# Kernel tuning notes

Hardware: AMD Instinct MI355X
Metric: run time of the kernel (lower is better)

## Reference

```python
import jax, jax.numpy as jnp
import numpy as np

N = 65536      # total nodes (64 graphs x 1024 nodes)
E = 1048576    # total edges
B = 64         # graphs in the batch
H = 128        # in_dim == hidden_dim
HEAD = 4
EPS = 1e-5


def setup_inputs() -> dict:
    key = jax.random.key(0)
    ks = jax.random.split(key, 16)
    s = 0.02
    return {
        "h": jax.random.normal(ks[0], (N, H), jnp.float32),
        "inter_f": jax.random.normal(ks[1], (B, H), jnp.float32),
        "gamma1": jnp.ones((H,), jnp.float32), "beta1": jnp.zeros((H,), jnp.float32),
        "W1": jax.random.normal(ks[2], (H, H), jnp.float32) * s, "b1": jnp.zeros((H,), jnp.float32),
        "gamma2": jnp.ones((H,), jnp.float32), "beta2": jnp.zeros((H,), jnp.float32),
        "W2": jax.random.normal(ks[3], (H, H), jnp.float32) * s, "b2": jnp.zeros((H,), jnp.float32),
        "Wq": jax.random.normal(ks[4], (HEAD, H, H), jnp.float32) * s,
        "Wk": jax.random.normal(ks[5], (HEAD, H, H), jnp.float32) * s,
        "Wv": jax.random.normal(ks[6], (HEAD, H, H), jnp.float32) * s,
        "Wc": jax.random.normal(ks[7], (HEAD * H, H), jnp.float32) * s,
        "ln_g": jnp.ones((H,), jnp.float32), "ln_b": jnp.zeros((H,), jnp.float32),
        "Wf1": jax.random.normal(ks[8], (H, 2 * H), jnp.float32) * s, "bf1": jnp.zeros((2 * H,), jnp.float32),
        "Wf2": jax.random.normal(ks[9], (2 * H, H), jnp.float32) * s, "bf2": jnp.zeros((H,), jnp.float32),
        "src": jax.random.randint(ks[10], (E,), 0, N, jnp.int32),
        "dst": jax.random.randint(ks[11], (E,), 0, N, jnp.int32),
        "graph_id": (jnp.arange(N) // (N // B)).astype(jnp.int32),
    }


def _bn(x, g, b):
    # BatchNorm1d (training-mode batch statistics, biased var)
    m = x.mean(0)
    v = jnp.mean((x - m) ** 2, 0)
    return (x - m) * jax.lax.rsqrt(v + EPS) * g + b


def _ln(x, g, b):
    m = x.mean(-1, keepdims=True)
    v = jnp.mean((x - m) ** 2, -1, keepdims=True)
    return (x - m) * jax.lax.rsqrt(v + EPS) * g + b


def _gconv(x, W, b, src, dst):
    # dgl GraphConv, norm='both': D_out^{-1/2} gather -> scatter-add -> D_in^{-1/2}, then W, b
    ones_e = jnp.ones((E,), x.dtype)
    dout = jnp.maximum(jax.ops.segment_sum(ones_e, src, num_segments=N), 1.0)
    din = jnp.maximum(jax.ops.segment_sum(ones_e, dst, num_segments=N), 1.0)
    msg = (x * jax.lax.rsqrt(dout)[:, None])[src]            # [E, H] gather
    agg = jax.ops.segment_sum(msg, dst, num_segments=N)      # [N, H] scatter-add
    agg = agg * jax.lax.rsqrt(din)[:, None]
    return agg @ W + b


def _forward(h, inter_f, gamma1, beta1, W1, b1, gamma2, beta2, W2, b2,
             Wq, Wk, Wv, Wc, ln_g, ln_b, Wf1, bf1, Wf2, bf2, src, dst, graph_id):
    # init pooling (mean_nodes)
    counts = jax.ops.segment_sum(jnp.ones((N,), h.dtype), graph_id, num_segments=B)
    init_avg_h = jax.ops.segment_sum(h, graph_id, num_segments=B) / counts[:, None]

    # two residual GraphConv blocks (dropout is identity at inference)
    h1 = h + jax.nn.relu(_gconv(_bn(h, gamma1, beta1), W1, b1, src, dst))
    h2 = h1 + jax.nn.relu(_gconv(_bn(h1, gamma2, beta2), W2, b2, src, dst))

    # broadcast_nodes(inter_f)
    inter_h = inter_f[graph_id]                               # [N, H]

    # transformer_block: per-head q/k/v, per-node scalar att, per-graph segment softmax
    q = jnp.einsum('nd,hdo->hno', h2, Wq)
    k = jnp.einsum('nd,hdo->hno', inter_h, Wk)
    v = jnp.einsum('nd,hdo->hno', h2, Wv)
    att = jnp.sum(q * k, axis=-1) / jnp.sqrt(jnp.float32(1280.0))   # [HEAD, N]
    mx = jax.vmap(lambda a: jax.ops.segment_max(a, graph_id, num_segments=B))(att)  # [HEAD, B]
    e = jnp.exp(att - mx[:, graph_id])
    ssum = jax.vmap(lambda a: jax.ops.segment_sum(a, graph_id, num_segments=B))(e)
    alpha = e / ssum[:, graph_id]                             # segment softmax per head
    tp = v * alpha[..., None]                                 # [HEAD, N, H]
    mo = tp.transpose(1, 0, 2).reshape(N, HEAD * H) @ Wc      # concat heads + project

    x1 = _ln(mo + h2, ln_g, ln_b)
    x2 = _ln(jax.nn.relu(x1 @ Wf1 + bf1) @ Wf2 + bf2 + x1, ln_g, ln_b)

    readout = jax.ops.segment_sum(x2, graph_id, num_segments=B)     # sum_nodes
    return readout, init_avg_h


def reference(h, inter_f, gamma1, beta1, W1, b1, gamma2, beta2, W2, b2,
              Wq, Wk, Wv, Wc, ln_g, ln_b, Wf1, bf1, Wf2, bf2, src, dst, graph_id):
    return _forward(h, inter_f, gamma1, beta1, W1, b1, gamma2, beta2, W2, b2,
                    Wq, Wk, Wv, Wc, ln_g, ln_b, Wf1, bf1, Wf2, bf2, src, dst, graph_id)
```

## Files before the change

kernel.cpp:

```cpp
#include <hip/hip_runtime.h>

#define NN 65536
#define NE 1048576
#define NB 64
#define HD 128
#define HD2 256
#define NHEAD 4
#define NPG 1024
#define BEPS 1e-5f
#define BM 64
#define ESTRIDE 20480

typedef short bf16x8s __attribute__((ext_vector_type(8)));
typedef float f32x4 __attribute__((ext_vector_type(4)));
#define MFMA16(a,b,c) __builtin_amdgcn_mfma_f32_16x16x32_bf16(a,b,c,0,0,0)

__device__ __forceinline__ unsigned short f2bf(float f) {
    union { float f; unsigned int u; } x{f};
    unsigned int r = x.u + 0x7FFFu + ((x.u >> 16) & 1u);
    return (unsigned short)(r >> 16);
}
__device__ __forceinline__ float b2f(unsigned short s) {
    union { unsigned int u; float f; } x{((unsigned int)s) << 16};
    return x.f;
}

__global__ __launch_bounds__(1024) void k_prep_pool(const int* __restrict__ src, const int* __restrict__ dst,
                                                    int* __restrict__ gcurD, int* __restrict__ gcurS,
                                                    unsigned int* __restrict__ dbuck, unsigned short* __restrict__ sbuck,
                                                    const float* __restrict__ h,
                                                    float* __restrict__ psum, float* __restrict__ psq) {
    const int t = threadIdx.x;
    if (blockIdx.x < 64) {
        __shared__ int cntD[64], cntS[64], baseD[64], baseS[64];
        if (t < 64) { cntD[t] = 0; cntS[t] = 0; }
        __syncthreads();
        const int e0 = blockIdx.x * 16384;
        int sv[16], dv[16];
        #pragma unroll
        for (int j = 0; j < 16; ++j) {
            int e = e0 + j * 1024 + t;
            sv[j] = src[e]; dv[j] = dst[e];
            atomicAdd(&cntD[dv[j] >> 10], 1);
            atomicAdd(&cntS[sv[j] >> 10], 1);
        }
        __syncthreads();
        if (t < 64) baseD[t] = atomicAdd(&gcurD[t * 32], cntD[t]);
        else if (t < 128) baseS[t - 64] = atomicAdd(&gcurS[(t - 64) * 32], cntS[t - 64]);
        __syncthreads();
        if (t < 64) { cntD[t] = 0; cntS[t] = 0; }
        __syncthreads();
        #pragma unroll
        for (int j = 0; j < 16; ++j) {
            int gd = dv[j] >> 10;
            int slot = baseD[gd] + atomicAdd(&cntD[gd], 1);
            if (slot < ESTRIDE)
                dbuck[gd * ESTRIDE + slot] = (unsigned)(dv[j] & 1023) | ((unsigned)sv[j] << 10);
            int gs = sv[j] >> 10;
            int slot2 = baseS[gs] + atomicAdd(&cntS[gs], 1);
            if (slot2 < ESTRIDE)
                sbuck[gs * ESTRIDE + slot2] = (unsigned short)(sv[j] & 1023);
        }
    } else {
        __shared__ float ls[1024], lq[1024];
        const int bb = blockIdx.x - 64;
        const int r0 = bb * 256;
        const int c = t & 127, strip8 = t >> 7;
        float s = 0.f, sq = 0.f;
        for (int i = 0; i < 32; ++i) {
            float v = h[(size_t)(r0 + strip8 * 32 + i) * HD + c];
            s += v; sq += v * v;
        }
        ls[t] = s; lq[t] = sq;
        __syncthreads();
        if (t < 128) {
            float ss = 0.f, qq = 0.f;
            #pragma unroll
            for (int k = 0; k < 8; ++k) { ss += ls[t + k * 128]; qq += lq[t + k * 128]; }
            psum[bb * HD + t] = ss;
            psq[bb * HD + t]  = qq;
        }
    }
}

__global__ __launch_bounds__(1024) void k_prep2(const int* __restrict__ gcurD, const int* __restrict__ gcurS,
                                                const unsigned int* __restrict__ dbuck,
                                                const unsigned short* __restrict__ sbuck,
                                                float* __restrict__ din_r, float* __restrict__ dout_r,
                                                int* __restrict__ beg, int* __restrict__ endv,
                                                int* __restrict__ elist) {
    __shared__ int hist[1024];
    __shared__ int pre[1024];
    const int t = threadIdx.x;
    const int b = blockIdx.x;
    if (b < 64) {
        const int g = b;
        const int n = min(gcurD[g * 32], ESTRIDE);
        const unsigned int* pd = dbuck + g * ESTRIDE;
        hist[t] = 0;
        __syncthreads();
        for (int i = t; i < n; i += 1024) atomicAdd(&hist[pd[i] & 1023], 1);
        __syncthreads();
        const int cnt = hist[t];
        din_r[g * 1024 + t] = rsqrtf((float)max(cnt, 1));
        int x = cnt; pre[t] = x;
        __syncthreads();
        #pragma unroll
        for (int off = 1; off < 1024; off <<= 1) {
            int v = (t >= off) ? pre[t - off] : 0;
            __syncthreads();
            x += v; pre[t] = x;
            __syncthreads();
        }
        const int excl = x - cnt;
        beg[g * 1024 + t]  = g * ESTRIDE + excl;
        endv[g * 1024 + t] = g * ESTRIDE + excl + cnt;
        __syncthreads();
        hist[t] = excl; pre[t] = 0;
        __syncthreads();
        for (int i = t; i < n; i += 1024) {
            unsigned int w = pd[i];
            int dl = w & 1023;
            int r = atomicAdd(&pre[dl], 1);
            elist[g * ESTRIDE + hist[dl] + r] = (int)(w >> 10);
        }
    } else {
        const int g = b - 64;
        const int m = min(gcurS[g * 32], ESTRIDE);
        const unsigned short* ps = sbuck + g * ESTRIDE;
        hist[t] = 0;
        __syncthreads();
        for (int i = t; i < m; i += 1024) atomicAdd(&hist[ps[i]], 1);
        __syncthreads();
        dout_r[g * 1024 + t] = rsqrtf((float)max(hist[t], 1));
    }
}

__device__ __forceinline__ void dev_prepW(int idx, const float* __restrict__ W,
                                          unsigned short* __restrict__ frag, int O) {
    int l = idx & 63, tt = idx >> 6;
    int ot = O >> 4;
    int c = tt % ot, ks = tt / ot;
    int q = l >> 4, m = l & 15;
    const float* wp = W + (size_t)(ks * 32 + q * 8) * O + c * 16 + m;
    union { uint4 v; unsigned short u[8]; } pk;
    #pragma unroll
    for (int j = 0; j < 8; ++j) pk.u[j] = f2bf(wp[(size_t)j * O]);
    *(uint4*)(frag + (size_t)idx * 8) = pk.v;
}

__global__ __launch_bounds__(256) void k_wprep(const float* __restrict__ W1, const float* __restrict__ W2,
                                               const float* __restrict__ Wf1, const float* __restrict__ Wf2,
                                               const float* __restrict__ interf, const float* __restrict__ Wk,
                                               const float* __restrict__ Wq, const float* __restrict__ Wv,
                                               const float* __restrict__ Wc,
                                               unsigned short* __restrict__ W1f, unsigned short* __restrict__ W2f,
                                               unsigned short* __restrict__ Wf1f, unsigned short* __restrict__ Wf2f,
                                               float* __restrict__ watt, unsigned short* __restrict__ Uf,
                                               const float* __restrict__ psum, const float* __restrict__ psq,
                                               float* __restrict__ out_avg,
                                               float* __restrict__ colsum, float* __restrict__ colsq) {
    const int b = blockIdx.x, t = threadIdx.x;
    if (b < 8)        dev_prepW(b * 256 + t, W1, W1f, 128);
    else if (b < 16)  dev_prepW((b - 8) * 256 + t, W2, W2f, 128);
    else if (b < 32)  dev_prepW((b - 16) * 256 + t, Wf1, Wf1f, 256);
    else if (b < 48)  dev_prepW((b - 32) * 256 + t, Wf2, Wf2f, 128);
    else if (b < 304) {
        int hb = b - 48;
        int hh = hb >> 6, g = hb & 63;
        __shared__ float f[HD];
        __shared__ float kv[HD];
        if (t < HD) f[t] = interf[g * HD + t];
        __syncthreads();
        if (t < HD) {
            const float* Wkh = Wk + (size_t)hh * HD * HD;
            float s = 0.f;
            for (int d = 0; d < HD; ++d) s += f[d] * Wkh[(size_t)d * HD + t];
            kv[t] = s;
        }
        __syncthreads();
        if (t < HD) {
            const float* row = Wq + ((size_t)hh * HD + t) * HD;
            float s2 = 0.f;
            #pragma unroll 4
            for (int o = 0; o < HD; o += 4) {
                float4 w = *(const float4*)(row + o);
                s2 += w.x * kv[o] + w.y * kv[o + 1] + w.z * kv[o + 2] + w.w * kv[o + 3];
            }
            watt[hb * HD + t] = s2 * 0.027950849718747373f;
        }
    } else if (b < 560) {
        int idx = (b - 304) * 256 + t;
        int o = idx & 127;
        int d = (idx >> 7) & 127;
        int hh = idx >> 14;
        const float* wv = Wv + ((size_t)hh * HD + d) * HD;
        const float* wc = Wc + (size_t)(hh * HD) * HD + o;
        float s = 0.f;
        for (int m2 = 0; m2 < HD; ++m2) s += wv[m2] * wc[(size_t)m2 * HD];
        int ks = d >> 5, dd = d & 31, q = dd >> 3, j = dd & 7;
        int c = o >> 4, m = o & 15, l = q * 16 + m;
        Uf[(size_t)((((hh * 4 + ks) * 8 + c) * 64 + l) * 8 + j)] = f2bf(s);
    } else {
        const int col = b - 560;
        __shared__ float ls[256], lq[256];
        ls[t] = psum[t * HD + col];
        lq[t] = psq[t * HD + col];
        __syncthreads();
        if (t < 64) {
            float a4 = ls[4 * t] + ls[4 * t + 1] + ls[4 * t + 2] + ls[4 * t + 3];
            out_avg[t * HD + col] = a4 * (1.0f / NPG);
            float b4 = lq[4 * t] + lq[4 * t + 1] + lq[4 * t + 2] + lq[4 * t + 3];
            float ts = a4, tq = b4;
            #pragma unroll
            for (int mk = 1; mk <= 32; mk <<= 1) {
                ts += __shfl_xor(ts, mk, 64);
                tq += __shfl_xor(tq, mk, 64);
            }
            if (t == 0) { colsum[col] = ts; colsq[col] = tq; }
        }
    }
}

template<bool IN32>
__global__ __launch_bounds__(256) void k_bnpack(const void* __restrict__ xin,
                                                const float* __restrict__ colsum, const float* __restrict__ colsq,
                                                const float* __restrict__ gma, const float* __restrict__ bta,
                                                const float* __restrict__ dout_r, unsigned short* __restrict__ xn) {
    int idx = blockIdx.x * 256 + threadIdx.x;
    int node = idx >> 4;
    int c8 = (idx & 15) * 8;
    float sc[8], sh[8];
    #pragma unroll
    for (int j = 0; j < 8; ++j) {
        float mean = colsum[c8 + j] * (1.0f / NN);
        float var  = colsq[c8 + j] * (1.0f / NN) - mean * mean;
        float rstd = rsqrtf(var + BEPS);
        sc[j] = rstd * gma[c8 + j];
        sh[j] = bta[c8 + j] - mean * sc[j];
    }
    float dr = dout_r[node];
    float v[8];
    if (IN32) {
        const float* x = (const float*)xin;
        float4 v0 = *(const float4*)(x + (size_t)node * HD + c8);
        float4 v1 = *(const float4*)(x + (size_t)node * HD + c8 + 4);
        v[0] = v0.x; v[1] = v0.y; v[2] = v0.z; v[3] = v0.w;
        v[4] = v1.x; v[5] = v1.y; v[6] = v1.z; v[7] = v1.w;
    } else {
        const unsigned short* x = (const unsigned short*)xin;
        union { uint4 u; unsigned short s[8]; } r;
        r.u = *(const uint4*)(x + (size_t)node * HD + c8);
        #pragma unroll
        for (int j = 0; j < 8; ++j) v[j] = b2f(r.s[j]);
    }
    union { uint4 v; unsigned short u[8]; } pk;
    #pragma unroll
    for (int j = 0; j < 8; ++j) pk.u[j] = f2bf((v[j] * sc[j] + sh[j]) * dr);
    *(uint4*)(xn + (size_t)node * HD + c8) = pk.v;
}

__global__ __launch_bounds__(256) void k_aggregate(const unsigned short* __restrict__ xn,
                                                   const float* __restrict__ din_r,
                                                   const int* __restrict__ beg, const int* __restrict__ endv,
                                                   const int* __restrict__ elist,
                                                   unsigned short* __restrict__ agg) {
    const int tid = threadIdx.x;
    const int node = blockIdx.x * 4 + (tid >> 6);
    const int c2 = (tid & 63) * 2;
    const int b0 = beg[node], e0 = endv[node];
    float a0 = 0.f, a1 = 0.f;
    int i = b0;
    for (; i + 4 <= e0; i += 4) {
        int s0 = elist[i], s1 = elist[i + 1], s2 = elist[i + 2], s3 = elist[i + 3];
        unsigned int v0 = *(const unsigned int*)(xn + (size_t)s0 * HD + c2);
        unsigned int v1 = *(const unsigned int*)(xn + (size_t)s1 * HD + c2);
        unsigned int v2 = *(const unsigned int*)(xn + (size_t)s2 * HD + c2);
        unsigned int v3 = *(const unsigned int*)(xn + (size_t)s3 * HD + c2);
        a0 += b2f((unsigned short)v0) + b2f((unsigned short)v1) + b2f((unsigned short)v2) + b2f((unsigned short)v3);
        a1 += b2f((unsigned short)(v0 >> 16)) + b2f((unsigned short)(v1 >> 16))
            + b2f((unsigned short)(v2 >> 16)) + b2f((unsigned short)(v3 >> 16));
    }
    for (; i < e0; ++i) {
        int s = elist[i];
        unsigned int v = *(const unsigned int*)(xn + (size_t)s * HD + c2);
        a0 += b2f((unsigned short)v);
        a1 += b2f((unsigned short)(v >> 16));
    }
    float dn = din_r[node];
    ushort2 o;
    o.x = f2bf(a0 * dn); o.y = f2bf(a1 * dn);
    *(ushort2*)(agg + (size_t)node * HD + c2) = o;
}

template<bool SCORES, bool STATS, bool RES32>
__global__ __launch_bounds__(256) void k_gconv_mfma(const unsigned short* __restrict__ agg,
                                                    const unsigned short* __restrict__ Wfrag,
                                                    const float* __restrict__ bias,
                                                    const void* __restrict__ res, unsigned short* __restrict__ outp,
                                                    const float* __restrict__ watt, float* __restrict__ att,
                                                    float* __restrict__ part2s, float* __restrict__ part2q) {
    __shared__ float credS[4 * HD];
    __shared__ float credQ[4 * HD];
    const int tid = threadIdx.x;
    const int w = tid >> 6, l = tid & 63, q = l >> 4, m = l & 15;
    const int node = blockIdx.x * BM + w * 16 + m;
    bf16x8s a[4];
    #pragma unroll
    for (int ks = 0; ks < 4; ++ks)
        a[ks] = *(const bf16x8s*)(agg + (size_t)node * HD + ks * 32 + q * 8);
    f32x4 acc[8] = {};
    #pragma unroll
    for (int ks = 0; ks < 4; ++ks) {
        #pragma unroll
        for (int c = 0; c < 8; ++c) {
            bf16x8s b = *(const bf16x8s*)(Wfrag + (size_t)((ks * 8 + c) * 64 + l) * 8);
            acc[c] = MFMA16(b, a[ks], acc[c]);
        }
    }
    float vals[8][4];
    #pragma unroll
    for (int c = 0; c < 8; ++c) {
        const int col = c * 16 + q * 4;
        float4 bv = *(const float4*)(bias + col);
        float rv[4];
        if (RES32) {
            float4 r4 = *(const float4*)((const float*)res + (size_t)node * HD + col);
            rv[0] = r4.x; rv[1] = r4.y; rv[2] = r4.z; rv[3] = r4.w;
        } else {
            ushort4 r4 = *(const ushort4*)((const unsigned short*)res + (size_t)node * HD + col);
            rv[0] = b2f(r4.x); rv[1] = b2f(r4.y); rv[2] = b2f(r4.z); rv[3] = b2f(r4.w);
        }
        vals[c][0] = rv[0] + fmaxf(acc[c][0] + bv.x, 0.f);
        vals[c][1] = rv[1] + fmaxf(acc[c][1] + bv.y, 0.f);
        vals[c][2] = rv[2] + fmaxf(acc[c][2] + bv.z, 0.f);
        vals[c][3] = rv[3] + fmaxf(acc[c][3] + bv.w, 0.f);
        ushort4 o;
        o.x = f2bf(vals[c][0]); o.y = f2bf(vals[c][1]);
        o.z = f2bf(vals[c][2]); o.w = f2bf(vals[c][3]);
        *(ushort4*)(outp + (size_t)node * HD + col) = o;
    }
    if (SCORES) {
        const int g = node >> 10;
        #pragma unroll
        for (int hh = 0; hh < NHEAD; ++hh) {
            const float* wp = watt + ((size_t)(hh * NB + g)) * HD;
            float s = 0.f;
            #pragma unroll
            for (int c = 0; c < 8; ++c) {
                const int col = c * 16 + q * 4;
                float4 wv = *(const float4*)(wp + col);
                s += vals[c][0] * wv.x + vals[c][1] * wv.y + vals[c][2] * wv.z + vals[c][3] * wv.w;
            }
            s += __shfl_xor(s, 16, 64);
            s += __shfl_xor(s, 32, 64);
            if (q == 0) att[(size_t)hh * NN + node] = s;
        }
    }
    if (STATS) {
        #pragma unroll
        for (int c = 0; c < 8; ++c) {
            #pragma unroll
            for (int r = 0; r < 4; ++r) {
                float v = vals[c][r];
                float vq = v * v;
                #pragma unroll
                for (int mk = 1; mk <= 8; mk <<= 1) {
                    v  += __shfl_xor(v, mk, 64);
                    vq += __shfl_xor(vq, mk, 64);
                }
                if (m == 0) {
                    credS[w * HD + c * 16 + q * 4 + r] = v;
                    credQ[w * HD + c * 16 + q * 4 + r] = vq;
                }
            }
        }
        __syncthreads();
        if (tid < HD) {
            part2s[(size_t)blockIdx.x * HD + tid] =
                credS[tid] + credS[HD + tid] + credS[2 * HD + tid] + credS[3 * HD + tid];
            part2q[(size_t)blockIdx.x * HD + tid] =
                credQ[tid] + credQ[HD + tid] + credQ[2 * HD + tid] + credQ[3 * HD + tid];
        }
    }
}

__global__ __launch_bounds__(256) void k_red2(const float* __restrict__ part2s, const float* __restrict__ part2q,
                                              float* __restrict__ colsum, float* __restrict__ colsq) {
    __shared__ float ws[8];
    const int col = blockIdx.x, t = threadIdx.x;
    float s = 0.f, sq = 0.f;
    #pragma unroll
    for (int k = 0; k < 4; ++k) {
        s  += part2s[(size_t)(t + k * 256) * HD + col];
        sq += part2q[(size_t)(t + k * 256) * HD + col];
    }
    #pragma unroll
    for (int mk = 1; mk <= 32; mk <<= 1) {
        s  += __shfl_xor(s, mk, 64);
        sq += __shfl_xor(sq, mk, 64);
    }
    if ((t & 63) == 0) { ws[(t >> 6) * 2] = s; ws[(t >> 6) * 2 + 1] = sq; }
    __syncthreads();
    if (t == 0) colsum[col] = ws[0] + ws[2] + ws[4] + ws[6];
    if (t == 1) colsq[col]  = ws[1] + ws[3] + ws[5] + ws[7];
}

__global__ __launch_bounds__(256) void k_segsoftmax(const float* __restrict__ att, float* __restrict__ alpha) {
    const int hh = blockIdx.x >> 6, g = blockIdx.x & 63;
    const int t = threadIdx.x;
    const float* a = att + (size_t)hh * NN + g * NPG;
    float* al = alpha + (size_t)hh * NN + g * NPG;
    float v[4]; float mx = -1e30f;
    #pragma unroll
    for (int i = 0; i < 4; ++i) { v[i] = a[t + i * 256]; mx = fmaxf(mx, v[i]); }
    #pragma unroll
    for (int m = 32; m > 0; m >>= 1) mx = fmaxf(mx, __shfl_xor(mx, m, 64));
    __shared__ float redm[4], reds[4];
    if ((t & 63) == 0) redm[t >> 6] = mx;
    __syncthreads();
    mx = fmaxf(fmaxf(redm[0], redm[1]), fmaxf(redm[2], redm[3]));
    float s = 0.f;
    #pragma unroll
    for (int i = 0; i < 4; ++i) { v[i] = __expf(v[i] - mx); s += v[i]; }
    #pragma unroll
    for (int m = 32; m > 0; m >>= 1) s += __shfl_xor(s, m, 64);
    if ((t & 63) == 0) reds[t >> 6] = s;
    __syncthreads();
    s = reds[0] + reds[1] + reds[2] + reds[3];
    float inv = 1.f / s;
    #pragma unroll
    for (int i = 0; i < 4; ++i) al[t + i * 256] = v[i] * inv;
}

__global__ __launch_bounds__(256) void k_mo_x1(const unsigned short* __restrict__ h2b,
                                               const unsigned short* __restrict__ Ufrag,
                                               const float* __restrict__ alpha,
                                               const float* __restrict__ lng, const float* __restrict__ lnb,
                                               unsigned short* __restrict__ x1b) {
    const int tid = threadIdx.x;
    const int w = tid >> 6, l = tid & 63, q = l >> 4, m = l & 15;
    const int node = blockIdx.x * BM + w * 16 + m;
    bf16x8s a[4];
    #pragma unroll
    for (int ks = 0; ks < 4; ++ks)
        a[ks] = *(const bf16x8s*)(h2b + (size_t)node * HD + ks * 32 + q * 8);
    f32x4 mo[8] = {};
    #pragma unroll
    for (int hh = 0; hh < 4; ++hh) {
        f32x4 acc[8] = {};
        #pragma unroll
        for (int ks = 0; ks < 4; ++ks) {
            #pragma unroll
            for (int c = 0; c < 8; ++c) {
                bf16x8s b = *(const bf16x8s*)(Ufrag + (size_t)(((hh * 4 + ks) * 8 + c) * 64 + l) * 8);
                acc[c] = MFMA16(b, a[ks], acc[c]);
            }
        }
        float al = alpha[(size_t)hh * NN + node];
        #pragma unroll
        for (int c = 0; c < 8; ++c) {
            mo[c][0] += al * acc[c][0];
            mo[c][1] += al * acc[c][1];
            mo[c][2] += al * acc[c][2];
            mo[c][3] += al * acc[c][3];
        }
    }
    float vals[8][4]; float s = 0.f, sq = 0.f;
    #pragma unroll
    for (int c = 0; c < 8; ++c) {
        const int col = c * 16 + q * 4;
        ushort4 hv = *(const ushort4*)(h2b + (size_t)node * HD + col);
        vals[c][0] = mo[c][0] + b2f(hv.x);
        vals[c][1] = mo[c][1] + b2f(hv.y);
        vals[c][2] = mo[c][2] + b2f(hv.z);
        vals[c][3] = mo[c][3] + b2f(hv.w);
        #pragma unroll
        for (int r = 0; r < 4; ++r) { s += vals[c][r]; sq += vals[c][r] * vals[c][r]; }
    }
    s  += __shfl_xor(s, 16, 64);  s  += __shfl_xor(s, 32, 64);
    sq += __shfl_xor(sq, 16, 64); sq += __shfl_xor(sq, 32, 64);
    float mean = s * (1.f / HD);
    float var  = sq * (1.f / HD) - mean * mean;
    float rstd = rsqrtf(var + BEPS);
    #pragma unroll
    for (int c = 0; c < 8; ++c) {
        const int col = c * 16 + q * 4;
        float4 gv = *(const float4*)(lng + col);
        float4 bv = *(const float4*)(lnb + col);
        ushort4 o;
        o.x = f2bf((vals[c][0] - mean) * rstd * gv.x + bv.x);
        o.y = f2bf((vals[c][1] - mean) * rstd * gv.y + bv.y);
        o.z = f2bf((vals[c][2] - mean) * rstd * gv.z + bv.z);
        o.w = f2bf((vals[c][3] - mean) * rstd * gv.w + bv.w);
        *(ushort4*)(x1b + (size_t)node * HD + col) = o;
    }
}

__global__ __launch_bounds__(256) void k_ffn1_mfma(const unsigned short* __restrict__ x1b,
                                                   const unsigned short* __restrict__ Wfrag,
                                                   const float* __restrict__ bias,
                                                   unsigned short* __restrict__ mid) {
    const int tid = threadIdx.x;
    const int w = tid >> 6, l = tid & 63, q = l >> 4, m = l & 15;
    const int node = blockIdx.x * BM + w * 16 + m;
    bf16x8s a[4];
    #pragma unroll
    for (int ks = 0; ks < 4; ++ks)
        a[ks] = *(const bf16x8s*)(x1b + (size_t)node * HD + ks * 32 + q * 8);
    f32x4 acc[16] = {};
    #pragma unroll
    for (int ks = 0; ks < 4; ++ks) {
        #pragma unroll
        for (int c = 0; c < 16; ++c) {
            bf16x8s b = *(const bf16x8s*)(Wfrag + (size_t)((ks * 16 + c) * 64 + l) * 8);
            acc[c] = MFMA16(b, a[ks], acc[c]);
        }
    }
    #pragma unroll
    for (int c = 0; c < 16; ++c) {
        const int col = c * 16 + q * 4;
        float4 bv = *(const float4*)(bias + col);
        ushort4 o;
        o.x = f2bf(fmaxf(acc[c][0] + bv.x, 0.f));
        o.y = f2bf(fmaxf(acc[c][1] + bv.y, 0.f));
        o.z = f2bf(fmaxf(acc[c][2] + bv.z, 0.f));
        o.w = f2bf(fmaxf(acc[c][3] + bv.w, 0.f));
        *(ushort4*)(mid + (size_t)node * HD2 + col) = o;
    }
}

__global__ __launch_bounds__(256) void k_ffn2_mfma(const unsigned short* __restrict__ mid,
                                                   const unsigned short* __restrict__ Wfrag,
                                                   const float* __restrict__ bias,
                                                   const unsigned short* __restrict__ x1b,
                                                   const float* __restrict__ lng, const float* __restrict__ lnb,
                                                   float* __restrict__ rpart) {
    __shared__ float cred[4 * HD];
    const int tid = threadIdx.x;
    const int w = tid >> 6, l = tid & 63, q = l >> 4, m = l & 15;
    const int node = blockIdx.x * BM + w * 16 + m;
    bf16x8s a[8];
    #pragma unroll
    for (int ks = 0; ks < 8; ++ks)
        a[ks] = *(const bf16x8s*)(mid + (size_t)node * HD2 + ks * 32 + q * 8);
    f32x4 acc[8] = {};
    #pragma unroll
    for (int ks = 0; ks < 8; ++ks) {
        #pragma unroll
        for (int c = 0; c < 8; ++c) {
            bf16x8s b = *(const bf16x8s*)(Wfrag + (size_t)((ks * 8 + c) * 64 + l) * 8);
            acc[c] = MFMA16(b, a[ks], acc[c]);
        }
    }
    float vals[8][4]; float s = 0.f, sq = 0.f;
    #pragma unroll
    for (int c = 0; c < 8; ++c) {
        const int col = c * 16 + q * 4;
        float4 bv = *(const float4*)(bias + col);
        ushort4 xv = *(const ushort4*)(x1b + (size_t)node * HD + col);
        vals[c][0] = acc[c][0] + bv.x + b2f(xv.x);
        vals[c][1] = acc[c][1] + bv.y + b2f(xv.y);
        vals[c][2] = acc[c][2] + bv.z + b2f(xv.z);
        vals[c][3] = acc[c][3] + bv.w + b2f(xv.w);
        #pragma unroll
        for (int r = 0; r < 4; ++r) { s += vals[c][r]; sq += vals[c][r] * vals[c][r]; }
    }
    s  += __shfl_xor(s, 16, 64);  s  += __shfl_xor(s, 32, 64);
    sq += __shfl_xor(sq, 16, 64); sq += __shfl_xor(sq, 32, 64);
    float mean = s * (1.f / HD);
    float var  = sq * (1.f / HD) - mean * mean;
    float rstd = rsqrtf(var + BEPS);
    #pragma unroll
    for (int c = 0; c < 8; ++c) {
        const int col = c * 16 + q * 4;
        float4 gv = *(const float4*)(lng + col);
        float4 bv = *(const float4*)(lnb + col);
        float4 o;
        o.x = (vals[c][0] - mean) * rstd * gv.x + bv.x;
        o.y = (vals[c][1] - mean) * rstd * gv.y + bv.y;
        o.z = (vals[c][2] - mean) * rstd * gv.z + bv.z;
        o.w = (vals[c][3] - mean) * rstd * gv.w + bv.w;
        #pragma unroll
        for (int mk = 1; mk <= 8; mk <<= 1) {
            o.x += __shfl_xor(o.x, mk, 64);
            o.y += __shfl_xor(o.y, mk, 64);
            o.z += __shfl_xor(o.z, mk, 64);
            o.w += __shfl_xor(o.w, mk, 64);
        }
        if (m == 0) *(float4*)(cred + w * HD + col) = o;
    }
    __syncthreads();
    if (tid < HD)
        rpart[(size_t)blockIdx.x * HD + tid] =
            cred[tid] + cred[HD + tid] + cred[2 * HD + tid] + cred[3 * HD + tid];
}

__global__ __launch_bounds__(256) void k_redout(const float* __restrict__ rpart, float* __restrict__ outp) {
    __shared__ float ls[256];
    const int g = blockIdx.x, t = threadIdx.x;
    const int c = t & 127, half = t >> 7;
    float s = 0.f;
    #pragma unroll
    for (int k = 0; k < 8; ++k)
        s += rpart[(size_t)(g * 16 + half * 8 + k) * HD + c];
    ls[t] = s;
    __syncthreads();
    if (t < 128) outp[g * HD + t] = ls[t] + ls[t + 128];
}

extern "C" void kernel_launch(void* const* d_in, const int* in_sizes, int n_in,
                              void* d_out, int out_size, void* d_ws, size_t ws_size,
                              hipStream_t stream) {
    (void)in_sizes; (void)n_in; (void)out_size;
    const float* h      = (const float*)d_in[0];
    const float* interf = (const float*)d_in[1];
    const float* gamma1 = (const float*)d_in[2];
    const float* beta1  = (const float*)d_in[3];
    const float* W1     = (const float*)d_in[4];
    const float* b1     = (const float*)d_in[5];
    const float* gamma2 = (const float*)d_in[6];
    const float* beta2  = (const float*)d_in[7];
    const float* W2     = (const float*)d_in[8];
    const float* b2     = (const float*)d_in[9];
    const float* Wq     = (const float*)d_in[10];
    const float* Wk     = (const float*)d_in[11];
    const float* Wv     = (const float*)d_in[12];
    const float* Wc     = (const float*)d_in[13];
    const float* ln_g   = (const float*)d_in[14];
    const float* ln_b   = (const float*)d_in[15];
    const float* Wf1    = (const float*)d_in[16];
    const float* bf1    = (const float*)d_in[17];
    const float* Wf2    = (const float*)d_in[18];
    const float* bf2    = (const float*)d_in[19];
    const int*   src    = (const int*)d_in[20];
    const int*   dst    = (const int*)d_in[21];

    float* out = (float*)d_out;
    float* R1 = (float*)d_ws;
    float* R2 = R1 + 8388608;
    float* R3 = R2 + 8388608;
    float* aux = R3 + 8388608;

    unsigned int*   dbuck = (unsigned int*)R1;
    unsigned short* sbuck = (unsigned short*)(R1 + 1310720);
    unsigned short* h1b   = (unsigned short*)R1;
    unsigned short* x1b   = (unsigned short*)R1;
    int*   elist = (int*)R2;
    unsigned short* h2b   = (unsigned short*)R2;
    float* psum  = R2 + 4194304;
    float* psq   = R2 + 4227072;
    float* rpart = R2 + 4194304;
    unsigned short* xn   = (unsigned short*)R3;
    unsigned short* aggb = (unsigned short*)(R3 + 4194304);
    float* att    = R3;
    float* alpha  = R3 + 262144;
    float* part2s = R3 + 2097152;
    float* part2q = R3 + 2228224;
    unsigned short* mid = (unsigned short*)R3;

    float* dout_r  = aux;
    float* din_r   = aux + 65536;
    float* colsum1 = aux + 131072;
    float* colsq1  = aux + 131200;
    float* colsum2 = aux + 131328;
    float* colsq2  = aux + 131456;
    int*   gcurD   = (int*)(aux + 131584);
    int*   gcurS   = (int*)(aux + 133632);
    float* watt    = aux + 135680;
    int*   beg     = (int*)(aux + 168448);
    int*   endv    = (int*)(aux + 233984);
    unsigned short* W1f  = (unsigned short*)(aux + 299520);
    unsigned short* W2f  = (unsigned short*)(aux + 307712);
    unsigned short* Wf1f = (unsigned short*)(aux + 315904);
    unsigned short* Wf2f = (unsigned short*)(aux + 332288);
    unsigned short* Uf   = (unsigned short*)(aux + 348672);

    if (ws_size < (size_t)(25165824 + 381440) * 4) return;

    hipMemsetAsync(gcurD, 0, 4096 * sizeof(int), stream);

    k_prep_pool<<<320, 1024, 0, stream>>>(src, dst, gcurD, gcurS, dbuck, sbuck, h, psum, psq);
    k_prep2<<<128, 1024, 0, stream>>>(gcurD, gcurS, dbuck, sbuck, din_r, dout_r, beg, endv, elist);
    k_wprep<<<688, 256, 0, stream>>>(W1, W2, Wf1, Wf2, interf, Wk, Wq, Wv, Wc,
                                     W1f, W2f, Wf1f, Wf2f, watt, Uf,
                                     psum, psq, out + 8192, colsum1, colsq1);

    k_bnpack<true><<<4096, 256, 0, stream>>>(h, colsum1, colsq1, gamma1, beta1, dout_r, xn);
    k_aggregate<<<16384, 256, 0, stream>>>(xn, din_r, beg, endv, elist, aggb);
    k_gconv_mfma<false, true, true><<<1024, 256, 0, stream>>>(aggb, W1f, b1, h, h1b,
                                                              nullptr, nullptr, part2s, part2q);
    k_red2<<<128, 256, 0, stream>>>(part2s, part2q, colsum2, colsq2);

    k_bnpack<false><<<4096, 256, 0, stream>>>(h1b, colsum2, colsq2, gamma2, beta2, dout_r, xn);
    k_aggregate<<<16384, 256, 0, stream>>>(xn, din_r, beg, endv, elist, aggb);
    k_gconv_mfma<true, false, false><<<1024, 256, 0, stream>>>(aggb, W2f, b2, h1b, h2b,
                                                               watt, att, nullptr, nullptr);

    k_segsoftmax<<<256, 256, 0, stream>>>(att, alpha);
    k_mo_x1<<<1024, 256, 0, stream>>>(h2b, Uf, alpha, ln_g, ln_b, x1b);
    k_ffn1_mfma<<<1024, 256, 0, stream>>>(x1b, Wf1f, bf1, mid);
    k_ffn2_mfma<<<1024, 256, 0, stream>>>(mid, Wf2f, bf2, x1b, ln_g, ln_b, rpart);
    k_redout<<<64, 256, 0, stream>>>(rpart, out);
}
```

Baseline: 292.1 us.

## Split aggregation across column chunks and edge groups, shrink edge list to ushort

The CSR edge list now stores source node ids as 16-bit values, halving its footprint. The neighbour aggregation kernel is remapped: instead of one wavefront walking all edges of a node over all 128 columns, each wavefront handles a 16-column chunk. Eight edge groups of eight lanes process edges in parallel and are combined with cross-lane shuffle reductions. The grid grows eightfold to cover the column chunks. This aims to cut the serial dependency chain per node and expose more memory-level parallelism. In exchange, each row read shrinks to a 32-byte segment, and the edge list and row cache lines are re-fetched once per chunk.

```diff
diff --git a/kernel.cpp b/kernel.cpp
--- a/kernel.cpp
+++ b/kernel.cpp
@@ -88,7 +88,7 @@
                                                 const unsigned short* __restrict__ sbuck,
                                                 float* __restrict__ din_r, float* __restrict__ dout_r,
                                                 int* __restrict__ beg, int* __restrict__ endv,
-                                                int* __restrict__ elist) {
+                                                unsigned short* __restrict__ elist) {
     __shared__ int hist[1024];
     __shared__ int pre[1024];
     const int t = threadIdx.x;
@@ -122,7 +122,7 @@
             unsigned int w = pd[i];
             int dl = w & 1023;
             int r = atomicAdd(&pre[dl], 1);
-            elist[g * ESTRIDE + hist[dl] + r] = (int)(w >> 10);
+            elist[g * ESTRIDE + hist[dl] + r] = (unsigned short)(w >> 10);
         }
     } else {
         const int g = b - 64;
@@ -263,34 +263,33 @@
 __global__ __launch_bounds__(256) void k_aggregate(const unsigned short* __restrict__ xn,
                                                    const float* __restrict__ din_r,
                                                    const int* __restrict__ beg, const int* __restrict__ endv,
-                                                   const int* __restrict__ elist,
+                                                   const unsigned short* __restrict__ elist,
                                                    unsigned short* __restrict__ agg) {
     const int tid = threadIdx.x;
-    const int node = blockIdx.x * 4 + (tid >> 6);
-    const int c2 = (tid & 63) * 2;
+    const int b = blockIdx.x;
+    const int chunk = b >> 14;
+    const int inner = b & 16383;
+    const int node = inner * 4 + (tid >> 6);
+    const int lane = tid & 63;
+    const int egrp = lane >> 3;
+    const int cc = chunk * 16 + (lane & 7) * 2;
     const int b0 = beg[node], e0 = endv[node];
     float a0 = 0.f, a1 = 0.f;
-    int i = b0;
-    for (; i + 4 <= e0; i += 4) {
-        int s0 = elist[i], s1 = elist[i + 1], s2 = elist[i + 2], s3 = elist[i + 3];
-        unsigned int v0 = *(const unsigned int*)(xn + (size_t)s0 * HD + c2);
-        unsigned int v1 = *(const unsigned int*)(xn + (size_t)s1 * HD + c2);
-        unsigned int v2 = *(const unsigned int*)(xn + (size_t)s2 * HD + c2);
-        unsigned int v3 = *(const unsigned int*)(xn + (size_t)s3 * HD + c2);
-        a0 += b2f((unsigned short)v0) + b2f((unsigned short)v1) + b2f((unsigned short)v2) + b2f((unsigned short)v3);
-        a1 += b2f((unsigned short)(v0 >> 16)) + b2f((unsigned short)(v1 >> 16))
-            + b2f((unsigned short)(v2 >> 16)) + b2f((unsigned short)(v3 >> 16));
-    }
-    for (; i < e0; ++i) {
+    for (int i = b0 + egrp; i < e0; i += 8) {
         int s = elist[i];
-        unsigned int v = *(const unsigned int*)(xn + (size_t)s * HD + c2);
+        unsigned int v = *(const unsigned int*)(xn + (size_t)s * HD + cc);
         a0 += b2f((unsigned short)v);
         a1 += b2f((unsigned short)(v >> 16));
     }
-    float dn = din_r[node];
-    ushort2 o;
-    o.x = f2bf(a0 * dn); o.y = f2bf(a1 * dn);
-    *(ushort2*)(agg + (size_t)node * HD + c2) = o;
+    a0 += __shfl_xor(a0, 8, 64);  a1 += __shfl_xor(a1, 8, 64);
+    a0 += __shfl_xor(a0, 16, 64); a1 += __shfl_xor(a1, 16, 64);
+    a0 += __shfl_xor(a0, 32, 64); a1 += __shfl_xor(a1, 32, 64);
+    if (egrp == 0) {
+        float dn = din_r[node];
+        ushort2 o;
+        o.x = f2bf(a0 * dn); o.y = f2bf(a1 * dn);
+        *(ushort2*)(agg + (size_t)node * HD + cc) = o;
+    }
 }
 
 template<bool SCORES, bool STATS, bool RES32>
@@ -646,7 +645,7 @@
     unsigned short* sbuck = (unsigned short*)(R1 + 1310720);
     unsigned short* h1b   = (unsigned short*)R1;
     unsigned short* x1b   = (unsigned short*)R1;
-    int*   elist = (int*)R2;
+    unsigned short* elist = (unsigned short*)R2;
     unsigned short* h2b   = (unsigned short*)R2;
     float* psum  = R2 + 4194304;
     float* psq   = R2 + 4227072;
@@ -687,13 +686,13 @@
                                      psum, psq, out + 8192, colsum1, colsq1);
 
     k_bnpack<true><<<4096, 256, 0, stream>>>(h, colsum1, colsq1, gamma1, beta1, dout_r, xn);
-    k_aggregate<<<16384, 256, 0, stream>>>(xn, din_r, beg, endv, elist, aggb);
+    k_aggregate<<<131072, 256, 0, stream>>>(xn, din_r, beg, endv, elist, aggb);
     k_gconv_mfma<false, true, true><<<1024, 256, 0, stream>>>(aggb, W1f, b1, h, h1b,
                                                               nullptr, nullptr, part2s, part2q);
     k_red2<<<128, 256, 0, stream>>>(part2s, part2q, colsum2, colsq2);
 
     k_bnpack<false><<<4096, 256, 0, stream>>>(h1b, colsum2, colsq2, gamma2, beta2, dout_r, xn);
-    k_aggregate<<<16384, 256, 0, stream>>>(xn, din_r, beg, endv, elist, aggb);
+    k_aggregate<<<131072, 256, 0, stream>>>(xn, din_r, beg, endv, elist, aggb);
     k_gconv_mfma<true, false, false><<<1024, 256, 0, stream>>>(aggb, W2f, b2, h1b, h2b,
                                                                watt, att, nullptr, nullptr);
 
```

New measurement: 571.5 us. 1.96x slower.

## Store CSR edge list as 16-bit, sort each row, unroll aggregation by 8

Applied to the files above, without the earlier changes.

Edge sources in the CSR list are narrowed from int32 to uint16 and staged in shared memory, and each destination's incoming-edge run is insertion-sorted so gathers walk source rows in ascending order for better cache locality. The aggregation loop gains an 8-way unrolled path to keep more independent gathers in flight. The per-thread serial insertion sort adds work to the prep kernel, and a 40 KB shared array lowers that kernel's occupancy. Narrowing to 16 bits assumes the source ids in each bucket fit in 16 bits, as the packing from the earlier bucketing step suggests.

```diff
diff --git a/kernel.cpp b/kernel.cpp
--- a/kernel.cpp
+++ b/kernel.cpp
@@ -88,9 +88,10 @@
                                                 const unsigned short* __restrict__ sbuck,
                                                 float* __restrict__ din_r, float* __restrict__ dout_r,
                                                 int* __restrict__ beg, int* __restrict__ endv,
-                                                int* __restrict__ elist) {
+                                                unsigned short* __restrict__ elist) {
     __shared__ int hist[1024];
     __shared__ int pre[1024];
+    __shared__ unsigned short lel[ESTRIDE];
     const int t = threadIdx.x;
     const int b = blockIdx.x;
     if (b < 64) {
@@ -122,8 +123,20 @@
             unsigned int w = pd[i];
             int dl = w & 1023;
             int r = atomicAdd(&pre[dl], 1);
-            elist[g * ESTRIDE + hist[dl] + r] = (int)(w >> 10);
-        }
+            lel[hist[dl] + r] = (unsigned short)(w >> 10);
+        }
+        __syncthreads();
+        {
+            unsigned short* run = lel + excl;
+            for (int a2 = 1; a2 < cnt; ++a2) {
+                unsigned short key = run[a2];
+                int p2 = a2 - 1;
+                while (p2 >= 0 && run[p2] > key) { run[p2 + 1] = run[p2]; --p2; }
+                run[p2 + 1] = key;
+            }
+        }
+        __syncthreads();
+        for (int i = t; i < n; i += 1024) elist[g * ESTRIDE + i] = lel[i];
     } else {
         const int g = b - 64;
         const int m = min(gcurS[g * 32], ESTRIDE);
@@ -263,7 +276,7 @@
 __global__ __launch_bounds__(256) void k_aggregate(const unsigned short* __restrict__ xn,
                                                    const float* __restrict__ din_r,
                                                    const int* __restrict__ beg, const int* __restrict__ endv,
-                                                   const int* __restrict__ elist,
+                                                   const unsigned short* __restrict__ elist,
                                                    unsigned short* __restrict__ agg) {
     const int tid = threadIdx.x;
     const int node = blockIdx.x * 4 + (tid >> 6);
@@ -271,6 +284,24 @@
     const int b0 = beg[node], e0 = endv[node];
     float a0 = 0.f, a1 = 0.f;
     int i = b0;
+    for (; i + 8 <= e0; i += 8) {
+        int s0 = elist[i],     s1 = elist[i + 1], s2 = elist[i + 2], s3 = elist[i + 3];
+        int s4 = elist[i + 4], s5 = elist[i + 5], s6 = elist[i + 6], s7 = elist[i + 7];
+        unsigned int v0 = *(const unsigned int*)(xn + (size_t)s0 * HD + c2);
+        unsigned int v1 = *(const unsigned int*)(xn + (size_t)s1 * HD + c2);
+        unsigned int v2 = *(const unsigned int*)(xn + (size_t)s2 * HD + c2);
+        unsigned int v3 = *(const unsigned int*)(xn + (size_t)s3 * HD + c2);
+        unsigned int v4 = *(const unsigned int*)(xn + (size_t)s4 * HD + c2);
+        unsigned int v5 = *(const unsigned int*)(xn + (size_t)s5 * HD + c2);
+        unsigned int v6 = *(const unsigned int*)(xn + (size_t)s6 * HD + c2);
+        unsigned int v7 = *(const unsigned int*)(xn + (size_t)s7 * HD + c2);
+        a0 += b2f((unsigned short)v0) + b2f((unsigned short)v1) + b2f((unsigned short)v2) + b2f((unsigned short)v3)
+            + b2f((unsigned short)v4) + b2f((unsigned short)v5) + b2f((unsigned short)v6) + b2f((unsigned short)v7);
+        a1 += b2f((unsigned short)(v0 >> 16)) + b2f((unsigned short)(v1 >> 16))
+            + b2f((unsigned short)(v2 >> 16)) + b2f((unsigned short)(v3 >> 16))
+            + b2f((unsigned short)(v4 >> 16)) + b2f((unsigned short)(v5 >> 16))
+            + b2f((unsigned short)(v6 >> 16)) + b2f((unsigned short)(v7 >> 16));
+    }
     for (; i + 4 <= e0; i += 4) {
         int s0 = elist[i], s1 = elist[i + 1], s2 = elist[i + 2], s3 = elist[i + 3];
         unsigned int v0 = *(const unsigned int*)(xn + (size_t)s0 * HD + c2);
@@ -646,7 +677,7 @@
     unsigned short* sbuck = (unsigned short*)(R1 + 1310720);
     unsigned short* h1b   = (unsigned short*)R1;
     unsigned short* x1b   = (unsigned short*)R1;
-    int*   elist = (int*)R2;
+    unsigned short* elist = (unsigned short*)R2;
     unsigned short* h2b   = (unsigned short*)R2;
     float* psum  = R2 + 4194304;
     float* psq   = R2 + 4227072;
```

Result: slower. 328.5 us (+12.5%).
